# Performance work log

Measured on AMD Instinct MI355X. Metric: run time of the kernel, lower is better.

Reference implementation:

```python
import jax, jax.numpy as jnp
import numpy as np

N = 65536      # active voxels
K = 27         # 3x3x3 SubM kernel taps
CIN = 4        # input voxel features (x,y,z,intensity)
C = 32         # stage-1 channels
NW = 2048      # number of attention windows
CAP = 32       # padded voxels per window (NW*CAP == N)
H = 2          # attention heads
HD = C // H    # head dim
R = 144        # quantized relative-position bins


def _subm_conv(feats, pairs, w):
    # spconv SubMConv3d as gather-scatter: pairs[k, i] = input voxel feeding
    # kernel tap k of output voxel i, or -1 if that neighbor is empty.
    valid = pairs >= 0                      # [K, N]
    idx = jnp.where(valid, pairs, 0)
    g = feats[idx] * valid[:, :, None].astype(feats.dtype)   # [K, N, Cin]
    return jnp.einsum('knc,kcd->nd', g, w)                    # [N, Cout]


def _bn_relu(x, g, b):
    # BatchNorm1d (eval, running stats folded) + ReLU
    return jax.nn.relu(x * g + b)


def _res_block(x, pairs, g1, b1, w1, g2, b2, w2):
    h = _bn_relu(x, g1, b1)
    h = _subm_conv(h, pairs, w1)
    h = _bn_relu(h, g2, b2)
    h = _subm_conv(h, pairs, w2)
    return x + h  # identity branch (in_ch == out_ch)


def _sphere_attention(x, win_idx, rel_idx, w_qkv, b_qkv, w_proj, b_proj, tq, tk, tv):
    xw = x[win_idx]                                           # [NW, CAP, C]
    qkv = (xw @ w_qkv + b_qkv).reshape(NW, CAP, 3, H, HD)
    q = qkv[:, :, 0] * (HD ** -0.5)
    k = qkv[:, :, 1]
    v = qkv[:, :, 2]
    scores = jnp.einsum('wihd,wjhd->whij', q, k)              # [NW, H, CAP, CAP]
    # quantized relative-position contributions (rel_query / rel_key)
    rq = tq[rel_idx]                                          # [NW, CAP, CAP, H, HD]
    rk = tk[rel_idx]
    scores = scores + jnp.einsum('wihd,wijhd->whij', q, rq)
    scores = scores + jnp.einsum('wjhd,wijhd->whij', k, rk)
    attn = jax.nn.softmax(scores, axis=-1)
    out = jnp.einsum('whij,wjhd->wihd', attn, v)
    out = out + jnp.einsum('whij,wijhd->wihd', attn, tv[rel_idx])  # rel_value
    out = out.reshape(NW, CAP, C) @ w_proj + b_proj
    # scatter windows back to the flat voxel list (win_idx is a permutation)
    y = jnp.zeros_like(x).at[win_idx.reshape(-1)].set(out.reshape(-1, C))
    return x + y  # residual (drop_path=0 in stage 1)


def setup_inputs() -> dict:
    key = jax.random.key(0)
    ks = jax.random.split(key, 16)
    feats = jax.random.normal(ks[0], (N, CIN), dtype=jnp.float32)
    pairs = jax.random.randint(ks[1], (K, N), 0, N, dtype=jnp.int32)
    drop = jax.random.uniform(ks[2], (K, N)) < 0.3
    pairs = jnp.where(drop, -1, pairs)
    pairs = pairs.at[K // 2].set(jnp.arange(N, dtype=jnp.int32))  # center tap = self
    win_idx = jax.random.permutation(ks[3], N).reshape(NW, CAP).astype(jnp.int32)
    rel_idx = jax.random.randint(ks[4], (NW, CAP, CAP), 0, R, dtype=jnp.int32)

    def w(k, shape, s=0.05):
        return jax.random.normal(k, shape, dtype=jnp.float32) * s

    wk = jax.random.split(ks[5], 12)
    inp = dict(feats=feats, pairs=pairs, win_idx=win_idx, rel_idx=rel_idx,
               w_in=w(wk[0], (K, CIN, C)),
               rb1_g1=jnp.ones((C,)), rb1_b1=jnp.zeros((C,)), rb1_w1=w(wk[1], (K, C, C)),
               rb1_g2=jnp.ones((C,)), rb1_b2=jnp.zeros((C,)), rb1_w2=w(wk[2], (K, C, C)),
               rb2_g1=jnp.ones((C,)), rb2_b1=jnp.zeros((C,)), rb2_w1=w(wk[3], (K, C, C)),
               rb2_g2=jnp.ones((C,)), rb2_b2=jnp.zeros((C,)), rb2_w2=w(wk[4], (K, C, C)),
               w_qkv=w(wk[5], (C, 3 * C), 0.1), b_qkv=jnp.zeros((3 * C,)),
               w_proj=w(wk[6], (C, C), 0.1), b_proj=jnp.zeros((C,)),
               tq=w(wk[7], (R, H, HD)), tk=w(wk[8], (R, H, HD)), tv=w(wk[9], (R, H, HD)))
    return inp


def reference(feats, pairs, win_idx, rel_idx, w_in,
              rb1_g1, rb1_b1, rb1_w1, rb1_g2, rb1_b2, rb1_w2,
              rb2_g1, rb2_b1, rb2_w1, rb2_g2, rb2_b2, rb2_w2,
              w_qkv, b_qkv, w_proj, b_proj, tq, tk, tv):
    x = _subm_conv(feats, pairs, w_in)                       # input_conv
    x = _res_block(x, pairs, rb1_g1, rb1_b1, rb1_w1, rb1_g2, rb1_b2, rb1_w2)
    x = _res_block(x, pairs, rb2_g1, rb2_b1, rb2_w1, rb2_g2, rb2_b2, rb2_w2)
    x = _sphere_attention(x, win_idx, rel_idx, w_qkv, b_qkv, w_proj, b_proj, tq, tk, tv)
    return x
```

## Files before the change

kernel.cpp:

```cpp
#include <hip/hip_runtime.h>

typedef unsigned short u16;
typedef unsigned int u32;

#define N_PTS 65536
#define KK 27
#define CIN 4
#define CC 32
#define NWIN 2048
#define CAP 32
#define NH 2
#define HD 16

typedef short s16x8 __attribute__((ext_vector_type(8)));
typedef float f32x4 __attribute__((ext_vector_type(4)));

__device__ __forceinline__ float bf2f(u16 h) { return __uint_as_float(((u32)h) << 16); }
__device__ __forceinline__ u16 f2bf(float f) {
    u32 u = __float_as_uint(f);
    u32 r = (u + 0x7FFFu + ((u >> 16) & 1u)) >> 16;
    return (u16)r;
}
__device__ __forceinline__ float ldany(const void* src, int i, bool isbf) {
    return isbf ? bf2f(((const u16*)src)[i]) : ((const float*)src)[i];
}
__device__ __forceinline__ u16 ldbf(const void* src, int i, bool isbf) {
    return isbf ? ((const u16*)src)[i] : f2bf(((const float*)src)[i]);
}
__device__ __forceinline__ void unp8(uint4 u, float* f) {
    f[0] = __uint_as_float(u.x << 16); f[1] = __uint_as_float(u.x & 0xffff0000u);
    f[2] = __uint_as_float(u.y << 16); f[3] = __uint_as_float(u.y & 0xffff0000u);
    f[4] = __uint_as_float(u.z << 16); f[5] = __uint_as_float(u.z & 0xffff0000u);
    f[6] = __uint_as_float(u.w << 16); f[7] = __uint_as_float(u.w & 0xffff0000u);
}

__global__ void detect_kernel(const u32* __restrict__ w, int* flag) {
    int t = threadIdx.x;
    int cnt = 0;
    for (int i = t; i < 4096; i += 256) {
        u32 e = (w[i] >> 7) & 0xFFu;
        cnt += (e >= 100 && e <= 140) ? 1 : 0;
    }
    __shared__ int red[256];
    red[t] = cnt;
    __syncthreads();
    for (int s = 128; s > 0; s >>= 1) {
        if (t < s) red[t] += red[t + s];
        __syncthreads();
    }
    if (t == 0) flag[0] = (red[0] > 2048) ? 1 : 0;
}

struct Ptrs { const void* p[24]; };

__global__ __launch_bounds__(256) void prep_all(
    Ptrs in, const int* __restrict__ flag,
    u16* __restrict__ fbf,
    u16* __restrict__ WpA1, u16* __restrict__ WpA2,
    u16* __restrict__ WpB1, u16* __restrict__ WpB2, u16* __restrict__ WpIN,
    u16* __restrict__ wqkvB, u16* __restrict__ wprojB,
    u16* __restrict__ tqb, u16* __restrict__ tkb, u16* __restrict__ tvb,
    float* __restrict__ Pf)
{
    bool isbf = flag[0] != 0;
    int seg = blockIdx.y;
    int i = blockIdx.x * 256 + threadIdx.x;
    if (seg == 0) {
        if (i < N_PTS * CIN) fbf[i] = ldbf(in.p[0], i, isbf);
        return;
    }
    if (seg <= 4) {
        if (i < 27648) {
            int e = i & 7, l = (i >> 3) & 63, dt = (i >> 9) & 1, k = i >> 10;
            const void* src = in.p[seg == 1 ? 7 : seg == 2 ? 10 : seg == 3 ? 13 : 16];
            u16* dst = seg == 1 ? WpA1 : seg == 2 ? WpA2 : seg == 3 ? WpB1 : WpB2;
            dst[i] = ldbf(src, k * 1024 + ((l >> 4) * 8 + e) * 32 + dt * 16 + (l & 15), isbf);
        }
        return;
    }
    if (seg == 5) {
        if (i < 4096) {
            int e = i & 7, l = (i >> 3) & 63, dt = (i >> 9) & 1, kk = i >> 10;
            int g = kk * 32 + (l >> 4) * 8 + e;
            int tp = g >> 2, c = g & 3;
            WpIN[i] = (tp < KK) ? ldbf(in.p[4], tp * 128 + c * 32 + dt * 16 + (l & 15), isbf) : (u16)0;
        }
        return;
    }
    if (seg == 6) {
        if (i < 3072) {
            int e = i & 7, l = (i >> 3) & 63, n = i >> 9;
            wqkvB[i] = ldbf(in.p[17], ((l >> 4) * 8 + e) * 96 + n * 16 + (l & 15), isbf);
        } else if (i < 4096) {
            int o2 = i - 3072;
            int e = o2 & 7, l = (o2 >> 3) & 63, n = o2 >> 9;
            wprojB[o2] = ldbf(in.p[19], ((l >> 4) * 8 + e) * 32 + n * 16 + (l & 15), isbf);
        }
        return;
    }
    if (seg == 7) {
        if (i < 4608)            tqb[i] = ldbf(in.p[21], i, isbf);
        else if (i < 9216)       tkb[i - 4608] = ldbf(in.p[22], i - 4608, isbf);
        else if (i < 13824)      tvb[i - 9216] = ldbf(in.p[23], i - 9216, isbf);
        return;
    }
    if (i < 256) {
        const int srcs[8] = {5, 6, 8, 9, 11, 12, 14, 15};
        Pf[i] = ldany(in.p[srcs[i >> 5]], i & 31, isbf);
    } else if (i < 352) {
        Pf[i] = ldany(in.p[18], i - 256, isbf);
    } else if (i < 384) {
        Pf[i] = ldany(in.p[20], i - 352, isbf);
    }
}

__global__ __launch_bounds__(256) void convin_mfma(
    const u16* __restrict__ fb, const int* __restrict__ pairs,
    const u16* __restrict__ Wp, const float* __restrict__ gb,
    float* __restrict__ xbuf, u16* __restrict__ act_out)
{
    int t = threadIdx.x;
    int wv = t >> 6, l = t & 63;
    int lr = l & 15, lg = l >> 4;
    int p0 = (blockIdx.x * 4 + wv) * 16;
    int rowaddr = p0 + lr;

    f32x4 acc0 = {0.f, 0.f, 0.f, 0.f}, acc1 = {0.f, 0.f, 0.f, 0.f};
#pragma unroll
    for (int kk = 0; kk < 4; kk++) {
        int t0 = kk * 8 + lg * 2;
        int ta = t0 < 26 ? t0 : 26;
        int tb = (t0 + 1) < 26 ? (t0 + 1) : 26;
        int ia = pairs[ta * N_PTS + rowaddr];
        int ib = pairs[tb * N_PTS + rowaddr];
        u32 ma = (t0 < KK && ia >= 0) ? 0xFFFFFFFFu : 0u;
        u32 mb = (t0 + 1 < KK && ib >= 0) ? 0xFFFFFFFFu : 0u;
        uint2 qa = *(const uint2*)(fb + (long)(ia < 0 ? 0 : ia) * CIN);
        uint2 qb = *(const uint2*)(fb + (long)(ib < 0 ? 0 : ib) * CIN);
        union { uint4 q; s16x8 v; } a;
        a.q = make_uint4(qa.x & ma, qa.y & ma, qb.x & mb, qb.y & mb);
        const s16x8* wb = (const s16x8*)Wp + kk * 128 + l;
        s16x8 b0 = wb[0];
        s16x8 b1 = wb[64];
        acc0 = __builtin_amdgcn_mfma_f32_16x16x32_bf16(a.v, b0, acc0, 0, 0, 0);
        acc1 = __builtin_amdgcn_mfma_f32_16x16x32_bf16(a.v, b1, acc1, 0, 0, 0);
    }
    float g0 = gb[lr], b0v = gb[32 + lr], g1 = gb[16 + lr], b1v = gb[48 + lr];
#pragma unroll
    for (int r = 0; r < 4; r++) {
        int row = p0 + lg * 4 + r;
        long o0 = (long)row * 32 + lr, o1 = o0 + 16;
        float v0 = acc0[r], v1 = acc1[r];
        xbuf[o0] = v0; xbuf[o1] = v1;
        act_out[o0] = f2bf(fmaxf(fmaf(v0, g0, b0v), 0.f));
        act_out[o1] = f2bf(fmaxf(fmaf(v1, g1, b1v), 0.f));
    }
}

template <int M>
__global__ __launch_bounds__(256) void conv32_mfma(
    const u16* __restrict__ act_in, const int* __restrict__ pairs,
    const u16* __restrict__ Wp, const float* __restrict__ gb,
    float* __restrict__ xbuf, u16* __restrict__ act_out)
{
    int t = threadIdx.x;
    int wv = t >> 6, l = t & 63;
    int lr = l & 15, lg = l >> 4;
    int p0 = (blockIdx.x * 4 + wv) * 16;
    int rowaddr = p0 + lr;

    int idx[KK];
#pragma unroll
    for (int k = 0; k < KK; k++) idx[k] = pairs[k * N_PTS + rowaddr];

    f32x4 acc0 = {0.f, 0.f, 0.f, 0.f}, acc1 = {0.f, 0.f, 0.f, 0.f};
#pragma unroll
    for (int k = 0; k < KK; k++) {
        const s16x8* wb = (const s16x8*)Wp + k * 128 + l;
        s16x8 b0 = wb[0];
        s16x8 b1 = wb[64];
        int ic = idx[k] < 0 ? 0 : idx[k];
        uint4 q = *(const uint4*)(act_in + (long)ic * CC + lg * 8);
        u32 msk = idx[k] >= 0 ? 0xFFFFFFFFu : 0u;
        q.x &= msk; q.y &= msk; q.z &= msk; q.w &= msk;
        union { uint4 q; s16x8 v; } a;
        a.q = q;
        acc0 = __builtin_amdgcn_mfma_f32_16x16x32_bf16(a.v, b0, acc0, 0, 0, 0);
        acc1 = __builtin_amdgcn_mfma_f32_16x16x32_bf16(a.v, b1, acc1, 0, 0, 0);
    }
    float g0 = 0.f, b0v = 0.f, g1 = 0.f, b1v = 0.f;
    if (M & 4) { g0 = gb[lr]; b0v = gb[32 + lr]; g1 = gb[16 + lr]; b1v = gb[48 + lr]; }
#pragma unroll
    for (int r = 0; r < 4; r++) {
        int row = p0 + lg * 4 + r;
        long o0 = (long)row * 32 + lr, o1 = o0 + 16;
        float v0 = acc0[r], v1 = acc1[r];
        if (M & 1) { v0 += xbuf[o0]; v1 += xbuf[o1]; }
        if (M & 2) { xbuf[o0] = v0; xbuf[o1] = v1; }
        if (M & 4) {
            act_out[o0] = f2bf(fmaxf(fmaf(v0, g0, b0v), 0.f));
            act_out[o1] = f2bf(fmaxf(fmaf(v1, g1, b1v), 0.f));
        }
    }
}

__global__ __launch_bounds__(256) void attn3_kernel(
    const float* __restrict__ x, const int* __restrict__ win_idx,
    const int* __restrict__ rel_idx,
    const u16* __restrict__ wqkvB, const u16* __restrict__ wprojB,
    const float* __restrict__ Pf,
    const u16* __restrict__ tqb, const u16* __restrict__ tkb, const u16* __restrict__ tvb,
    float* __restrict__ out)
{
    __shared__ float xw[CAP][CC + 1];
    __shared__ u16 qsb[CAP][40];
    __shared__ u16 ksb[CAP][40];
    __shared__ u16 vsT[CC][40];
    __shared__ float sc[NH][CAP][36];
    __shared__ float ot[CAP][36];
    __shared__ int ridx[CAP * CAP];
    __shared__ int widx[CAP];

    int w = blockIdx.x, t = threadIdx.x;
    int wv = t >> 6, l = t & 63, lr = l & 15, lg = l >> 4;

    if (t < CAP) widx[t] = win_idx[w * CAP + t];
    __syncthreads();

    for (int e = t; e < CAP * CC; e += 256) {
        int i = e >> 5, c = e & 31;
        xw[i][c] = x[(long)widx[i] * CC + c];
        ridx[e] = rel_idx[(long)w * CAP * CAP + e];
    }
    __syncthreads();

    {
        const float* bqkv = Pf + 256;
        for (int pi = wv; pi < 12; pi += 4) {
            int n = pi >> 1, m = pi & 1;
            union { s16x8 v; u16 h[8]; } a;
            const float* xr = &xw[m * 16 + lr][0];
#pragma unroll
            for (int e = 0; e < 8; e++) a.h[e] = f2bf(xr[lg * 8 + e]);
            s16x8 b = *(const s16x8*)(wqkvB + ((n * 64 + l) << 3));
            f32x4 acc = {0.f, 0.f, 0.f, 0.f};
            acc = __builtin_amdgcn_mfma_f32_16x16x32_bf16(a.v, b, acc, 0, 0, 0);
            int tt = n * 16 + lr;
            float bias = bqkv[tt];
#pragma unroll
            for (int r = 0; r < 4; r++) {
                int tok = m * 16 + lg * 4 + r;
                float v = acc[r] + bias;
                if (tt < 32)      qsb[tok][tt] = f2bf(v * 0.25f);
                else if (tt < 64) ksb[tok][tt - 32] = f2bf(v);
                else              vsT[tt - 64][tok] = f2bf(v);
            }
        }
    }
    __syncthreads();

    for (int pi = wv; pi < 8; pi += 4) {
        int h = pi >> 2, m = (pi >> 1) & 1, n = pi & 1;
        s16x8 a = {0, 0, 0, 0, 0, 0, 0, 0}, b = {0, 0, 0, 0, 0, 0, 0, 0};
        if (lg < 2) {
            a = *(const s16x8*)(&qsb[m * 16 + lr][h * 16 + lg * 8]);
            b = *(const s16x8*)(&ksb[n * 16 + lr][h * 16 + lg * 8]);
        }
        f32x4 acc = {0.f, 0.f, 0.f, 0.f};
        acc = __builtin_amdgcn_mfma_f32_16x16x32_bf16(a, b, acc, 0, 0, 0);
#pragma unroll
        for (int r = 0; r < 4; r++)
            sc[h][m * 16 + lg * 4 + r][n * 16 + lr] = acc[r];
    }
    __syncthreads();

    for (int e = t; e < NH * CAP * CAP; e += 256) {
        int h = e >> 10, i = (e >> 5) & 31, j = e & 31;
        int r = ridx[i * 32 + j];
        float qf[16], kf[16], tf[16], uf[16];
        unp8(*(const uint4*)(&qsb[i][h * 16]), qf);
        unp8(*(const uint4*)(&qsb[i][h * 16 + 8]), qf + 8);
        unp8(*(const uint4*)(&ksb[j][h * 16]), kf);
        unp8(*(const uint4*)(&ksb[j][h * 16 + 8]), kf + 8);
        unp8(*(const uint4*)(tqb + r * 32 + h * 16), tf);
        unp8(*(const uint4*)(tqb + r * 32 + h * 16 + 8), tf + 8);
        unp8(*(const uint4*)(tkb + r * 32 + h * 16), uf);
        unp8(*(const uint4*)(tkb + r * 32 + h * 16 + 8), uf + 8);
        float s = sc[h][i][j];
#pragma unroll
        for (int d = 0; d < 16; d++) {
            s = fmaf(qf[d], tf[d], s);
            s = fmaf(kf[d], uf[d], s);
        }
        sc[h][i][j] = s;
    }
    __syncthreads();

    {
        int rr = t >> 2, sub = t & 3;
        int h = rr >> 5, i = rr & 31, j0 = sub * 8;
        float pv[8];
        float m = -1e30f;
#pragma unroll
        for (int jj = 0; jj < 8; jj++) { pv[jj] = sc[h][i][j0 + jj]; m = fmaxf(m, pv[jj]); }
        m = fmaxf(m, __shfl_xor(m, 1));
        m = fmaxf(m, __shfl_xor(m, 2));
        float sum = 0.f;
#pragma unroll
        for (int jj = 0; jj < 8; jj++) { pv[jj] = __expf(pv[jj] - m); sum += pv[jj]; }
        sum += __shfl_xor(sum, 1);
        sum += __shfl_xor(sum, 2);
        float inv = 1.f / sum;
#pragma unroll
        for (int jj = 0; jj < 8; jj++) sc[h][i][j0 + jj] = pv[jj] * inv;
    }
    __syncthreads();

    for (int o = t; o < CAP * 16; o += 256) {
        int i = o >> 4, hp = o & 15;
        int h = hp >> 3;
        float a0 = 0.f, a1 = 0.f;
#pragma unroll 8
        for (int j = 0; j < CAP; j++) {
            int r = ridx[i * 32 + j];
            float p = sc[h][i][j];
            u32 tv2 = *(const u32*)(tvb + r * 32 + hp * 2);
            a0 = fmaf(p, __uint_as_float(tv2 << 16), a0);
            a1 = fmaf(p, __uint_as_float(tv2 & 0xffff0000u), a1);
        }
        ot[i][hp * 2] = a0;
        ot[i][hp * 2 + 1] = a1;
    }
    __syncthreads();

    {
        int h = wv >> 1, m = wv & 1;
        union { s16x8 v; u16 hh[8]; } pa;
        const float* pr = &sc[h][m * 16 + lr][0];
#pragma unroll
        for (int e = 0; e < 8; e++) pa.hh[e] = f2bf(pr[lg * 8 + e]);
        s16x8 b = *(const s16x8*)(&vsT[h * 16 + lr][lg * 8]);
        f32x4 acc = {0.f, 0.f, 0.f, 0.f};
        acc = __builtin_amdgcn_mfma_f32_16x16x32_bf16(pa.v, b, acc, 0, 0, 0);
#pragma unroll
        for (int r = 0; r < 4; r++)
            ot[m * 16 + lg * 4 + r][h * 16 + lr] += acc[r];
    }
    __syncthreads();

    {
        int m = wv >> 1, n = wv & 1;
        union { s16x8 v; u16 hh[8]; } a;
        const float* orow = &ot[m * 16 + lr][0];
#pragma unroll
        for (int e = 0; e < 8; e++) a.hh[e] = f2bf(orow[lg * 8 + e]);
        s16x8 b = *(const s16x8*)(wprojB + ((n * 64 + l) << 3));
        f32x4 acc = {0.f, 0.f, 0.f, 0.f};
        acc = __builtin_amdgcn_mfma_f32_16x16x32_bf16(a.v, b, acc, 0, 0, 0);
        int c = n * 16 + lr;
        float bb = Pf[352 + c];
#pragma unroll
        for (int r = 0; r < 4; r++) {
            int tok = m * 16 + lg * 4 + r;
            out[(long)widx[tok] * CC + c] = xw[tok][c] + bb + acc[r];
        }
    }
}

#define B_PF     0
#define B_FLAG   1536
#define B_ACTA   2048
#define B_ACTB   4196352
#define B_FEATS  8390656
#define B_WA1    8914944
#define B_WA2    8970240
#define B_WB1    9025536
#define B_WB2    9080832
#define B_WIN    9136128
#define B_WQKVB  9144320
#define B_WPROJB 9150464
#define B_TQB    9152512
#define B_TKB    9161728
#define B_TVB    9170944

extern "C" void kernel_launch(void* const* d_in, const int* in_sizes, int n_in,
                              void* d_out, int out_size, void* d_ws, size_t ws_size,
                              hipStream_t stream) {
    const void* feats  = d_in[0];
    const int* pairs   = (const int*)d_in[1];
    const int* win_idx = (const int*)d_in[2];
    const int* rel_idx = (const int*)d_in[3];

    char* wsb = (char*)d_ws;
    float* Pf = (float*)(wsb + B_PF);
    int* flag = (int*)(wsb + B_FLAG);
    u16* actA = (u16*)(wsb + B_ACTA);
    u16* actB = (u16*)(wsb + B_ACTB);
    u16* fbf  = (u16*)(wsb + B_FEATS);
    u16* WpA1 = (u16*)(wsb + B_WA1);
    u16* WpA2 = (u16*)(wsb + B_WA2);
    u16* WpB1 = (u16*)(wsb + B_WB1);
    u16* WpB2 = (u16*)(wsb + B_WB2);
    u16* WpIN = (u16*)(wsb + B_WIN);
    u16* wqkvB  = (u16*)(wsb + B_WQKVB);
    u16* wprojB = (u16*)(wsb + B_WPROJB);
    u16* tqb = (u16*)(wsb + B_TQB);
    u16* tkb = (u16*)(wsb + B_TKB);
    u16* tvb = (u16*)(wsb + B_TVB);
    float* X  = (float*)d_out;

    detect_kernel<<<1, 256, 0, stream>>>((const u32*)feats, flag);

    Ptrs pp;
    for (int i = 0; i < 24; i++) pp.p[i] = d_in[i];
    prep_all<<<dim3(1024, 9), 256, 0, stream>>>(pp, flag, fbf,
                                                WpA1, WpA2, WpB1, WpB2, WpIN,
                                                wqkvB, wprojB, tqb, tkb, tvb, Pf);

    convin_mfma<<<1024, 256, 0, stream>>>(fbf, pairs, WpIN, Pf + 0, X, actA);
    conv32_mfma<4><<<1024, 256, 0, stream>>>(actA, pairs, WpA1, Pf + 64,  X, actB);
    conv32_mfma<7><<<1024, 256, 0, stream>>>(actB, pairs, WpA2, Pf + 128, X, actA);
    conv32_mfma<4><<<1024, 256, 0, stream>>>(actA, pairs, WpB1, Pf + 192, X, actB);
    conv32_mfma<3><<<1024, 256, 0, stream>>>(actB, pairs, WpB2, Pf, X, actA);

    attn3_kernel<<<NWIN, 256, 0, stream>>>(X, win_idx, rel_idx,
                                           wqkvB, wprojB, Pf,
                                           tqb, tkb, tvb, X);
}
```

Baseline: 136.2 us.

## Split conv kernel taps across waves and move rel-pos attention terms to MFMA

The sparse conv kernels now give each 16-row tile to a whole block, with the 27 taps split across four waves and the partial sums reduced through shared memory. That raises the number of blocks fourfold and spreads the latency of the gathers. The attention kernel now computes the relative-position query and key terms as MFMA products against all 144 bins followed by a gather, instead of per-element dot products. The relative value term becomes an atomic scatter into per-bin histograms followed by an MFMA against a re-laid-out tv table. These changes add synchronisation, shared-memory atomics and extra bf16 rounding of intermediate results.

```diff
diff --git a/kernel.cpp b/kernel.cpp
--- a/kernel.cpp
+++ b/kernel.cpp
@@ -27,12 +27,6 @@
 __device__ __forceinline__ u16 ldbf(const void* src, int i, bool isbf) {
     return isbf ? ((const u16*)src)[i] : f2bf(((const float*)src)[i]);
 }
-__device__ __forceinline__ void unp8(uint4 u, float* f) {
-    f[0] = __uint_as_float(u.x << 16); f[1] = __uint_as_float(u.x & 0xffff0000u);
-    f[2] = __uint_as_float(u.y << 16); f[3] = __uint_as_float(u.y & 0xffff0000u);
-    f[4] = __uint_as_float(u.z << 16); f[5] = __uint_as_float(u.z & 0xffff0000u);
-    f[6] = __uint_as_float(u.w << 16); f[7] = __uint_as_float(u.w & 0xffff0000u);
-}
 
 __global__ void detect_kernel(const u32* __restrict__ w, int* flag) {
     int t = threadIdx.x;
@@ -59,7 +53,7 @@
     u16* __restrict__ WpA1, u16* __restrict__ WpA2,
     u16* __restrict__ WpB1, u16* __restrict__ WpB2, u16* __restrict__ WpIN,
     u16* __restrict__ wqkvB, u16* __restrict__ wprojB,
-    u16* __restrict__ tqb, u16* __restrict__ tkb, u16* __restrict__ tvb,
+    u16* __restrict__ tqB, u16* __restrict__ tkB, u16* __restrict__ tvB,
     float* __restrict__ Pf)
 {
     bool isbf = flag[0] != 0;
@@ -99,9 +93,24 @@
         return;
     }
     if (seg == 7) {
-        if (i < 4608)            tqb[i] = ldbf(in.p[21], i, isbf);
-        else if (i < 9216)       tkb[i - 4608] = ldbf(in.p[22], i - 4608, isbf);
-        else if (i < 13824)      tvb[i - 9216] = ldbf(in.p[23], i - 9216, isbf);
+        if (i < 9216) {
+            int e = i & 7, l = (i >> 3) & 63, nn = i >> 9;
+            int n = nn % 9, h = nn / 9, lr = l & 15, lg = l >> 4;
+            int k = lg * 8 + e;
+            tqB[i] = (k < HD) ? ldbf(in.p[21], (n * 16 + lr) * 32 + h * 16 + k, isbf) : (u16)0;
+        } else if (i < 18432) {
+            int o2 = i - 9216;
+            int e = o2 & 7, l = (o2 >> 3) & 63, nn = o2 >> 9;
+            int n = nn % 9, h = nn / 9, lr = l & 15, lg = l >> 4;
+            int k = lg * 8 + e;
+            tkB[o2] = (k < HD) ? ldbf(in.p[22], (n * 16 + lr) * 32 + h * 16 + k, isbf) : (u16)0;
+        } else if (i < 23552) {
+            int o2 = i - 18432;
+            int e = o2 & 7, l = (o2 >> 3) & 63, kk2 = o2 >> 9;
+            int ks = kk2 % 5, h = kk2 / 5, lr = l & 15, lg = l >> 4;
+            int r = ks * 32 + lg * 8 + e;
+            tvB[o2] = (r < 144) ? ldbf(in.p[23], r * 32 + h * 16 + lr, isbf) : (u16)0;
+        }
         return;
     }
     if (i < 256) {
@@ -114,21 +123,19 @@
     }
 }
 
-__global__ __launch_bounds__(256) void convin_mfma(
+__global__ __launch_bounds__(256) void convin_s(
     const u16* __restrict__ fb, const int* __restrict__ pairs,
     const u16* __restrict__ Wp, const float* __restrict__ gb,
     float* __restrict__ xbuf, u16* __restrict__ act_out)
 {
-    int t = threadIdx.x;
-    int wv = t >> 6, l = t & 63;
-    int lr = l & 15, lg = l >> 4;
-    int p0 = (blockIdx.x * 4 + wv) * 16;
+    __shared__ float red[4][16][32];
+    int t = threadIdx.x, wv = t >> 6, l = t & 63, lr = l & 15, lg = l >> 4;
+    int p0 = blockIdx.x * 16;
     int rowaddr = p0 + lr;
 
     f32x4 acc0 = {0.f, 0.f, 0.f, 0.f}, acc1 = {0.f, 0.f, 0.f, 0.f};
-#pragma unroll
-    for (int kk = 0; kk < 4; kk++) {
-        int t0 = kk * 8 + lg * 2;
+    {
+        int t0 = wv * 8 + lg * 2;
         int ta = t0 < 26 ? t0 : 26;
         int tb = (t0 + 1) < 26 ? (t0 + 1) : 26;
         int ia = pairs[ta * N_PTS + rowaddr];
@@ -139,87 +146,113 @@
         uint2 qb = *(const uint2*)(fb + (long)(ib < 0 ? 0 : ib) * CIN);
         union { uint4 q; s16x8 v; } a;
         a.q = make_uint4(qa.x & ma, qa.y & ma, qb.x & mb, qb.y & mb);
-        const s16x8* wb = (const s16x8*)Wp + kk * 128 + l;
+        const s16x8* wb = (const s16x8*)Wp + wv * 128 + l;
         s16x8 b0 = wb[0];
         s16x8 b1 = wb[64];
         acc0 = __builtin_amdgcn_mfma_f32_16x16x32_bf16(a.v, b0, acc0, 0, 0, 0);
         acc1 = __builtin_amdgcn_mfma_f32_16x16x32_bf16(a.v, b1, acc1, 0, 0, 0);
     }
-    float g0 = gb[lr], b0v = gb[32 + lr], g1 = gb[16 + lr], b1v = gb[48 + lr];
 #pragma unroll
     for (int r = 0; r < 4; r++) {
-        int row = p0 + lg * 4 + r;
-        long o0 = (long)row * 32 + lr, o1 = o0 + 16;
-        float v0 = acc0[r], v1 = acc1[r];
-        xbuf[o0] = v0; xbuf[o1] = v1;
-        act_out[o0] = f2bf(fmaxf(fmaf(v0, g0, b0v), 0.f));
-        act_out[o1] = f2bf(fmaxf(fmaf(v1, g1, b1v), 0.f));
+        red[wv][lg * 4 + r][lr] = acc0[r];
+        red[wv][lg * 4 + r][lr + 16] = acc1[r];
+    }
+    __syncthreads();
+#pragma unroll
+    for (int e = t; e < 512; e += 256) {
+        int row = e >> 5, c = e & 31;
+        float v = red[0][row][c] + red[1][row][c] + red[2][row][c] + red[3][row][c];
+        long o = (long)(p0 + row) * 32 + c;
+        xbuf[o] = v;
+        act_out[o] = f2bf(fmaxf(fmaf(v, gb[c], gb[32 + c]), 0.f));
     }
 }
 
 template <int M>
-__global__ __launch_bounds__(256) void conv32_mfma(
+__global__ __launch_bounds__(256) void conv32s_mfma(
     const u16* __restrict__ act_in, const int* __restrict__ pairs,
     const u16* __restrict__ Wp, const float* __restrict__ gb,
     float* __restrict__ xbuf, u16* __restrict__ act_out)
 {
-    int t = threadIdx.x;
-    int wv = t >> 6, l = t & 63;
-    int lr = l & 15, lg = l >> 4;
-    int p0 = (blockIdx.x * 4 + wv) * 16;
+    __shared__ float red[4][16][32];
+    int t = threadIdx.x, wv = t >> 6, l = t & 63, lr = l & 15, lg = l >> 4;
+    int p0 = blockIdx.x * 16;
     int rowaddr = p0 + lr;
-
-    int idx[KK];
-#pragma unroll
-    for (int k = 0; k < KK; k++) idx[k] = pairs[k * N_PTS + rowaddr];
-
+    int k0 = wv * 7;
+
+    int idx[7];
+#pragma unroll
+    for (int q = 0; q < 7; q++) {
+        int k = k0 + q;
+        idx[q] = (k < KK) ? pairs[k * N_PTS + rowaddr] : -1;
+    }
     f32x4 acc0 = {0.f, 0.f, 0.f, 0.f}, acc1 = {0.f, 0.f, 0.f, 0.f};
 #pragma unroll
-    for (int k = 0; k < KK; k++) {
+    for (int q = 0; q < 7; q++) {
+        int k = k0 + q;
+        if (k >= KK) break;
         const s16x8* wb = (const s16x8*)Wp + k * 128 + l;
         s16x8 b0 = wb[0];
         s16x8 b1 = wb[64];
-        int ic = idx[k] < 0 ? 0 : idx[k];
-        uint4 q = *(const uint4*)(act_in + (long)ic * CC + lg * 8);
-        u32 msk = idx[k] >= 0 ? 0xFFFFFFFFu : 0u;
-        q.x &= msk; q.y &= msk; q.z &= msk; q.w &= msk;
+        int ic = idx[q] < 0 ? 0 : idx[q];
+        uint4 qv = *(const uint4*)(act_in + (long)ic * CC + lg * 8);
+        u32 msk = idx[q] >= 0 ? 0xFFFFFFFFu : 0u;
+        qv.x &= msk; qv.y &= msk; qv.z &= msk; qv.w &= msk;
         union { uint4 q; s16x8 v; } a;
-        a.q = q;
+        a.q = qv;
         acc0 = __builtin_amdgcn_mfma_f32_16x16x32_bf16(a.v, b0, acc0, 0, 0, 0);
         acc1 = __builtin_amdgcn_mfma_f32_16x16x32_bf16(a.v, b1, acc1, 0, 0, 0);
     }
-    float g0 = 0.f, b0v = 0.f, g1 = 0.f, b1v = 0.f;
-    if (M & 4) { g0 = gb[lr]; b0v = gb[32 + lr]; g1 = gb[16 + lr]; b1v = gb[48 + lr]; }
 #pragma unroll
     for (int r = 0; r < 4; r++) {
-        int row = p0 + lg * 4 + r;
-        long o0 = (long)row * 32 + lr, o1 = o0 + 16;
-        float v0 = acc0[r], v1 = acc1[r];
-        if (M & 1) { v0 += xbuf[o0]; v1 += xbuf[o1]; }
-        if (M & 2) { xbuf[o0] = v0; xbuf[o1] = v1; }
-        if (M & 4) {
-            act_out[o0] = f2bf(fmaxf(fmaf(v0, g0, b0v), 0.f));
-            act_out[o1] = f2bf(fmaxf(fmaf(v1, g1, b1v), 0.f));
-        }
-    }
-}
-
-__global__ __launch_bounds__(256) void attn3_kernel(
+        red[wv][lg * 4 + r][lr] = acc0[r];
+        red[wv][lg * 4 + r][lr + 16] = acc1[r];
+    }
+    __syncthreads();
+#pragma unroll
+    for (int e = t; e < 512; e += 256) {
+        int row = e >> 5, c = e & 31;
+        float v = red[0][row][c] + red[1][row][c] + red[2][row][c] + red[3][row][c];
+        long o = (long)(p0 + row) * 32 + c;
+        if (M & 1) v += xbuf[o];
+        if (M & 2) xbuf[o] = v;
+        if (M & 4) act_out[o] = f2bf(fmaxf(fmaf(v, gb[c], gb[32 + c]), 0.f));
+    }
+}
+
+#define A_XW    0
+#define A_RIDX  4224
+#define A_QSB   8320
+#define A_KSB   10880
+#define A_VST   13440
+#define A_SC    16000
+#define A_OTB   26240
+#define A_BIG   28800
+#define A_WIDX  49280
+#define A_SIZE  49408
+
+__global__ __launch_bounds__(256) void attn4_kernel(
     const float* __restrict__ x, const int* __restrict__ win_idx,
     const int* __restrict__ rel_idx,
     const u16* __restrict__ wqkvB, const u16* __restrict__ wprojB,
     const float* __restrict__ Pf,
-    const u16* __restrict__ tqb, const u16* __restrict__ tkb, const u16* __restrict__ tvb,
+    const u16* __restrict__ tqB, const u16* __restrict__ tkB, const u16* __restrict__ tvB,
     float* __restrict__ out)
 {
-    __shared__ float xw[CAP][CC + 1];
-    __shared__ u16 qsb[CAP][40];
-    __shared__ u16 ksb[CAP][40];
-    __shared__ u16 vsT[CC][40];
-    __shared__ float sc[NH][CAP][36];
-    __shared__ float ot[CAP][36];
-    __shared__ int ridx[CAP * CAP];
-    __shared__ int widx[CAP];
+    __shared__ __align__(16) char arena[A_SIZE];
+    float* xw   = (float*)(arena + A_XW);
+    int*   ridx = (int*)(arena + A_RIDX);
+    u16*   qsb  = (u16*)(arena + A_QSB);
+    u16*   ksb  = (u16*)(arena + A_KSB);
+    u16*   vsT  = (u16*)(arena + A_VST);
+    float* sc   = (float*)(arena + A_SC);
+    u16*   psb  = (u16*)(arena + A_SC);
+    u16*   otb  = (u16*)(arena + A_OTB);
+    u16*   Bq   = (u16*)(arena + A_BIG);
+    u16*   Bk   = (u16*)(arena + A_BIG) + 5120;
+    float* S    = (float*)(arena + A_BIG);
+    u16*   Sb   = (u16*)(arena + A_BIG);
+    int*   widx = (int*)(arena + A_WIDX);
 
     int w = blockIdx.x, t = threadIdx.x;
     int wv = t >> 6, l = t & 63, lr = l & 15, lg = l >> 4;
@@ -229,8 +262,8 @@
 
     for (int e = t; e < CAP * CC; e += 256) {
         int i = e >> 5, c = e & 31;
-        xw[i][c] = x[(long)widx[i] * CC + c];
-        ridx[e] = rel_idx[(long)w * CAP * CAP + e];
+        xw[i * 33 + c] = x[(long)widx[i] * CC + c];
+        ridx[e] = rel_idx[(long)w * 1024 + e];
     }
     __syncthreads();
 
@@ -239,7 +272,7 @@
         for (int pi = wv; pi < 12; pi += 4) {
             int n = pi >> 1, m = pi & 1;
             union { s16x8 v; u16 h[8]; } a;
-            const float* xr = &xw[m * 16 + lr][0];
+            const float* xr = xw + (m * 16 + lr) * 33;
 #pragma unroll
             for (int e = 0; e < 8; e++) a.h[e] = f2bf(xr[lg * 8 + e]);
             s16x8 b = *(const s16x8*)(wqkvB + ((n * 64 + l) << 3));
@@ -251,9 +284,9 @@
             for (int r = 0; r < 4; r++) {
                 int tok = m * 16 + lg * 4 + r;
                 float v = acc[r] + bias;
-                if (tt < 32)      qsb[tok][tt] = f2bf(v * 0.25f);
-                else if (tt < 64) ksb[tok][tt - 32] = f2bf(v);
-                else              vsT[tt - 64][tok] = f2bf(v);
+                if (tt < 32)      qsb[tok * 40 + tt] = f2bf(v * 0.25f);
+                else if (tt < 64) ksb[tok * 40 + (tt - 32)] = f2bf(v);
+                else              vsT[(tt - 64) * 40 + tok] = f2bf(v);
             }
         }
     }
@@ -263,106 +296,112 @@
         int h = pi >> 2, m = (pi >> 1) & 1, n = pi & 1;
         s16x8 a = {0, 0, 0, 0, 0, 0, 0, 0}, b = {0, 0, 0, 0, 0, 0, 0, 0};
         if (lg < 2) {
-            a = *(const s16x8*)(&qsb[m * 16 + lr][h * 16 + lg * 8]);
-            b = *(const s16x8*)(&ksb[n * 16 + lr][h * 16 + lg * 8]);
+            a = *(const s16x8*)(qsb + (m * 16 + lr) * 40 + h * 16 + lg * 8);
+            b = *(const s16x8*)(ksb + (n * 16 + lr) * 40 + h * 16 + lg * 8);
         }
         f32x4 acc = {0.f, 0.f, 0.f, 0.f};
         acc = __builtin_amdgcn_mfma_f32_16x16x32_bf16(a, b, acc, 0, 0, 0);
 #pragma unroll
         for (int r = 0; r < 4; r++)
-            sc[h][m * 16 + lg * 4 + r][n * 16 + lr] = acc[r];
-    }
-    __syncthreads();
-
-    for (int e = t; e < NH * CAP * CAP; e += 256) {
-        int h = e >> 10, i = (e >> 5) & 31, j = e & 31;
-        int r = ridx[i * 32 + j];
-        float qf[16], kf[16], tf[16], uf[16];
-        unp8(*(const uint4*)(&qsb[i][h * 16]), qf);
-        unp8(*(const uint4*)(&qsb[i][h * 16 + 8]), qf + 8);
-        unp8(*(const uint4*)(&ksb[j][h * 16]), kf);
-        unp8(*(const uint4*)(&ksb[j][h * 16 + 8]), kf + 8);
-        unp8(*(const uint4*)(tqb + r * 32 + h * 16), tf);
-        unp8(*(const uint4*)(tqb + r * 32 + h * 16 + 8), tf + 8);
-        unp8(*(const uint4*)(tkb + r * 32 + h * 16), uf);
-        unp8(*(const uint4*)(tkb + r * 32 + h * 16 + 8), uf + 8);
-        float s = sc[h][i][j];
-#pragma unroll
-        for (int d = 0; d < 16; d++) {
-            s = fmaf(qf[d], tf[d], s);
-            s = fmaf(kf[d], uf[d], s);
-        }
-        sc[h][i][j] = s;
-    }
-    __syncthreads();
+            sc[h * 1280 + (m * 16 + lg * 4 + r) * 40 + n * 16 + lr] = acc[r];
+    }
+    __syncthreads();
+
+    for (int h = 0; h < NH; h++) {
+        for (int pi = wv; pi < 36; pi += 4) {
+            int tb = pi >= 18 ? 1 : 0;
+            int rem = pi - tb * 18;
+            int m = rem / 9, n = rem % 9;
+            const u16* src = tb ? ksb : qsb;
+            const u16* tab = tb ? tkB : tqB;
+            s16x8 a = {0, 0, 0, 0, 0, 0, 0, 0};
+            if (lg < 2) a = *(const s16x8*)(src + (m * 16 + lr) * 40 + h * 16 + lg * 8);
+            s16x8 b = *(const s16x8*)(tab + (((h * 9 + n) * 64 + l) << 3));
+            f32x4 acc = {0.f, 0.f, 0.f, 0.f};
+            acc = __builtin_amdgcn_mfma_f32_16x16x32_bf16(a, b, acc, 0, 0, 0);
+            u16* dst = tb ? Bk : Bq;
+#pragma unroll
+            for (int r = 0; r < 4; r++)
+                dst[(m * 16 + lg * 4 + r) * 160 + n * 16 + lr] = f2bf(acc[r]);
+        }
+        __syncthreads();
+        for (int e = t; e < 1024; e += 256) {
+            int i = e >> 5, j = e & 31, r = ridx[e];
+            sc[h * 1280 + i * 40 + j] += bf2f(Bq[i * 160 + r]) + bf2f(Bk[j * 160 + r]);
+        }
+        __syncthreads();
+    }
 
     {
         int rr = t >> 2, sub = t & 3;
         int h = rr >> 5, i = rr & 31, j0 = sub * 8;
+        const float* srow = sc + h * 1280 + i * 40 + j0;
         float pv[8];
-        float m = -1e30f;
-#pragma unroll
-        for (int jj = 0; jj < 8; jj++) { pv[jj] = sc[h][i][j0 + jj]; m = fmaxf(m, pv[jj]); }
-        m = fmaxf(m, __shfl_xor(m, 1));
-        m = fmaxf(m, __shfl_xor(m, 2));
+        float m_ = -1e30f;
+#pragma unroll
+        for (int jj = 0; jj < 8; jj++) { pv[jj] = srow[jj]; m_ = fmaxf(m_, pv[jj]); }
+        m_ = fmaxf(m_, __shfl_xor(m_, 1));
+        m_ = fmaxf(m_, __shfl_xor(m_, 2));
         float sum = 0.f;
 #pragma unroll
-        for (int jj = 0; jj < 8; jj++) { pv[jj] = __expf(pv[jj] - m); sum += pv[jj]; }
+        for (int jj = 0; jj < 8; jj++) { pv[jj] = __expf(pv[jj] - m_); sum += pv[jj]; }
         sum += __shfl_xor(sum, 1);
         sum += __shfl_xor(sum, 2);
         float inv = 1.f / sum;
-#pragma unroll
-        for (int jj = 0; jj < 8; jj++) sc[h][i][j0 + jj] = pv[jj] * inv;
-    }
-    __syncthreads();
-
-    for (int o = t; o < CAP * 16; o += 256) {
-        int i = o >> 4, hp = o & 15;
-        int h = hp >> 3;
-        float a0 = 0.f, a1 = 0.f;
-#pragma unroll 8
-        for (int j = 0; j < CAP; j++) {
-            int r = ridx[i * 32 + j];
-            float p = sc[h][i][j];
-            u32 tv2 = *(const u32*)(tvb + r * 32 + hp * 2);
-            a0 = fmaf(p, __uint_as_float(tv2 << 16), a0);
-            a1 = fmaf(p, __uint_as_float(tv2 & 0xffff0000u), a1);
-        }
-        ot[i][hp * 2] = a0;
-        ot[i][hp * 2 + 1] = a1;
-    }
-    __syncthreads();
-
-    {
-        int h = wv >> 1, m = wv & 1;
-        union { s16x8 v; u16 hh[8]; } pa;
-        const float* pr = &sc[h][m * 16 + lr][0];
-#pragma unroll
-        for (int e = 0; e < 8; e++) pa.hh[e] = f2bf(pr[lg * 8 + e]);
-        s16x8 b = *(const s16x8*)(&vsT[h * 16 + lr][lg * 8]);
-        f32x4 acc = {0.f, 0.f, 0.f, 0.f};
-        acc = __builtin_amdgcn_mfma_f32_16x16x32_bf16(pa.v, b, acc, 0, 0, 0);
-#pragma unroll
-        for (int r = 0; r < 4; r++)
-            ot[m * 16 + lg * 4 + r][h * 16 + lr] += acc[r];
-    }
-    __syncthreads();
+        __syncthreads();
+        u16* prow = psb + h * 1280 + i * 40 + j0;
+#pragma unroll
+        for (int jj = 0; jj < 8; jj++) prow[jj] = f2bf(pv[jj] * inv);
+    }
+    __syncthreads();
+
+    for (int h = 0; h < NH; h++) {
+        for (int e = t; e < 5120; e += 256) S[e] = 0.f;
+        __syncthreads();
+        for (int e = t; e < 1024; e += 256) {
+            int i = e >> 5, j = e & 31, r = ridx[e];
+            float p = bf2f(psb[h * 1280 + i * 40 + j]);
+            atomicAdd(&S[i * 160 + r], p);
+        }
+        __syncthreads();
+        float tmp[20];
+#pragma unroll
+        for (int q = 0; q < 20; q++) tmp[q] = S[t + q * 256];
+        __syncthreads();
+#pragma unroll
+        for (int q = 0; q < 20; q++) Sb[t + q * 256] = f2bf(tmp[q]);
+        __syncthreads();
+        if ((wv >> 1) == h) {
+            int m = wv & 1;
+            f32x4 acc = {0.f, 0.f, 0.f, 0.f};
+            s16x8 a = *(const s16x8*)(psb + h * 1280 + (m * 16 + lr) * 40 + lg * 8);
+            s16x8 b = *(const s16x8*)(vsT + (h * 16 + lr) * 40 + lg * 8);
+            acc = __builtin_amdgcn_mfma_f32_16x16x32_bf16(a, b, acc, 0, 0, 0);
+#pragma unroll
+            for (int ks = 0; ks < 5; ks++) {
+                s16x8 a2 = *(const s16x8*)(Sb + (m * 16 + lr) * 160 + ks * 32 + lg * 8);
+                s16x8 b2 = *(const s16x8*)(tvB + (((h * 5 + ks) * 64 + l) << 3));
+                acc = __builtin_amdgcn_mfma_f32_16x16x32_bf16(a2, b2, acc, 0, 0, 0);
+            }
+#pragma unroll
+            for (int r = 0; r < 4; r++)
+                otb[(m * 16 + lg * 4 + r) * 40 + h * 16 + lr] = f2bf(acc[r]);
+        }
+        __syncthreads();
+    }
 
     {
         int m = wv >> 1, n = wv & 1;
-        union { s16x8 v; u16 hh[8]; } a;
-        const float* orow = &ot[m * 16 + lr][0];
-#pragma unroll
-        for (int e = 0; e < 8; e++) a.hh[e] = f2bf(orow[lg * 8 + e]);
+        s16x8 a = *(const s16x8*)(otb + (m * 16 + lr) * 40 + lg * 8);
         s16x8 b = *(const s16x8*)(wprojB + ((n * 64 + l) << 3));
         f32x4 acc = {0.f, 0.f, 0.f, 0.f};
-        acc = __builtin_amdgcn_mfma_f32_16x16x32_bf16(a.v, b, acc, 0, 0, 0);
+        acc = __builtin_amdgcn_mfma_f32_16x16x32_bf16(a, b, acc, 0, 0, 0);
         int c = n * 16 + lr;
         float bb = Pf[352 + c];
 #pragma unroll
         for (int r = 0; r < 4; r++) {
             int tok = m * 16 + lg * 4 + r;
-            out[(long)widx[tok] * CC + c] = xw[tok][c] + bb + acc[r];
+            out[(long)widx[tok] * CC + c] = xw[tok * 33 + c] + bb + acc[r];
         }
     }
 }
@@ -379,9 +418,9 @@
 #define B_WIN    9136128
 #define B_WQKVB  9144320
 #define B_WPROJB 9150464
-#define B_TQB    9152512
-#define B_TKB    9161728
-#define B_TVB    9170944
+#define B_TQBF   9152512
+#define B_TKBF   9170944
+#define B_TVBF   9189376
 
 extern "C" void kernel_launch(void* const* d_in, const int* in_sizes, int n_in,
                               void* d_out, int out_size, void* d_ws, size_t ws_size,
@@ -404,9 +443,9 @@
     u16* WpIN = (u16*)(wsb + B_WIN);
     u16* wqkvB  = (u16*)(wsb + B_WQKVB);
     u16* wprojB = (u16*)(wsb + B_WPROJB);
-    u16* tqb = (u16*)(wsb + B_TQB);
-    u16* tkb = (u16*)(wsb + B_TKB);
-    u16* tvb = (u16*)(wsb + B_TVB);
+    u16* tqB = (u16*)(wsb + B_TQBF);
+    u16* tkB = (u16*)(wsb + B_TKBF);
+    u16* tvB = (u16*)(wsb + B_TVBF);
     float* X  = (float*)d_out;
 
     detect_kernel<<<1, 256, 0, stream>>>((const u32*)feats, flag);
@@ -415,15 +454,15 @@
     for (int i = 0; i < 24; i++) pp.p[i] = d_in[i];
     prep_all<<<dim3(1024, 9), 256, 0, stream>>>(pp, flag, fbf,
                                                 WpA1, WpA2, WpB1, WpB2, WpIN,
-                                                wqkvB, wprojB, tqb, tkb, tvb, Pf);
-
-    convin_mfma<<<1024, 256, 0, stream>>>(fbf, pairs, WpIN, Pf + 0, X, actA);
-    conv32_mfma<4><<<1024, 256, 0, stream>>>(actA, pairs, WpA1, Pf + 64,  X, actB);
-    conv32_mfma<7><<<1024, 256, 0, stream>>>(actB, pairs, WpA2, Pf + 128, X, actA);
-    conv32_mfma<4><<<1024, 256, 0, stream>>>(actA, pairs, WpB1, Pf + 192, X, actB);
-    conv32_mfma<3><<<1024, 256, 0, stream>>>(actB, pairs, WpB2, Pf, X, actA);
-
-    attn3_kernel<<<NWIN, 256, 0, stream>>>(X, win_idx, rel_idx,
+                                                wqkvB, wprojB, tqB, tkB, tvB, Pf);
+
+    convin_s<<<4096, 256, 0, stream>>>(fbf, pairs, WpIN, Pf + 0, X, actA);
+    conv32s_mfma<4><<<4096, 256, 0, stream>>>(actA, pairs, WpA1, Pf + 64,  X, actB);
+    conv32s_mfma<7><<<4096, 256, 0, stream>>>(actB, pairs, WpA2, Pf + 128, X, actA);
+    conv32s_mfma<4><<<4096, 256, 0, stream>>>(actA, pairs, WpB1, Pf + 192, X, actB);
+    conv32s_mfma<3><<<4096, 256, 0, stream>>>(actB, pairs, WpB2, Pf, X, actA);
+
+    attn4_kernel<<<NWIN, 256, 0, stream>>>(X, win_idx, rel_idx,
                                            wqkvB, wprojB, Pf,
-                                           tqb, tkb, tvb, X);
-}
+                                           tqB, tkB, tvB, X);
+}
```

New measurement: 168.4 us. 23.6% more time.
